# Kernel optimization log

Measured on AMD Instinct MI355X. Metric: run time of the kernel, lower is better.

## Reference

```python
import jax, jax.numpy as jnp
import numpy as np

B, R, C, NH = 8, 64, 256, 8
N = R * R            # 4096 tokens
HD = C // NH         # head dim 32
FF = 3               # focusing factor

def dwconv(x, w, b):
    # x: (B, C, H, W); w: (C, 1, kh, kw) depthwise
    y = jax.lax.conv_general_dilated(
        x, w, window_strides=(1, 1), padding='SAME',
        dimension_numbers=('NCHW', 'OIHW', 'NCHW'),
        feature_group_count=x.shape[1])
    return y + b[None, :, None, None]

def setup_inputs() -> dict:
    key = jax.random.key(0)
    ks = jax.random.split(key, 6)
    return {
        'qkv': jax.random.normal(ks[0], (3, B, N, C), jnp.float32),
        'pos_enc': jax.random.normal(ks[1], (1, N, C), jnp.float32) * 0.02,
        'scale': jax.random.normal(ks[2], (1, 1, C), jnp.float32) * 0.02,
        'w_v': jax.random.normal(ks[3], (C, 1, 3, 3), jnp.float32) * 0.1,
        'b_v': jnp.zeros((C,), jnp.float32),
        'w_dwc': jax.random.normal(ks[4], (HD, 1, 5, 5), jnp.float32) * 0.1,
        'b_dwc': jnp.zeros((HD,), jnp.float32),
    }

def reference(qkv, pos_enc, scale, w_v, b_v, w_dwc, b_dwc):
    q, k, v = qkv[0], qkv[1], qkv[2]          # each (B, N, C)
    # --- LePE: depthwise 3x3 conv on v over full channel dim ---
    v_img = v.transpose(0, 2, 1).reshape(B, C, R, R)
    lepe = dwconv(v_img, w_v, b_v)            # (B, C, R, R)
    lepe = lepe.reshape(B * NH, HD, N).transpose(0, 2, 1)   # (B*h, N, hd)
    v = v_img.reshape(B, C, N).transpose(0, 2, 1)           # (B, N, C)
    # --- focused kernelization ---
    k = k + pos_enc
    sc = jax.nn.softplus(scale)
    q = (jax.nn.relu(q) + 1e-6) / sc
    k = (jax.nn.relu(k) + 1e-6) / sc
    qn = jnp.linalg.norm(q, axis=-1, keepdims=True)
    kn = jnp.linalg.norm(k, axis=-1, keepdims=True)
    q = q ** FF
    k = k ** FF
    q = q / jnp.linalg.norm(q, axis=-1, keepdims=True) * qn
    k = k / jnp.linalg.norm(k, axis=-1, keepdims=True) * kn
    split = lambda x: x.reshape(B, N, NH, HD).transpose(0, 2, 1, 3).reshape(B * NH, N, HD)
    q, k, v = split(q), split(k), split(v)    # (B*h, N, hd)
    # --- linear attention (kv aggregation path: N >> hd) ---
    z = 1.0 / (jnp.einsum('bic,bc->bi', q, k.sum(axis=1)) + 1e-6)
    kv = jnp.einsum('bjc,bjd->bcd', k, v)     # (B*h, hd, hd)
    x = jnp.einsum('bic,bcd,bi->bid', q, kv, z)
    # --- dwc feature mixing on v per head ---
    fm = v.transpose(0, 2, 1).reshape(B * NH, HD, R, R)
    fm = dwconv(fm, w_dwc, b_dwc).reshape(B * NH, HD, N).transpose(0, 2, 1)
    x = x + fm + lepe
    x = x.reshape(B, NH, N, HD).transpose(0, 2, 1, 3).reshape(B, N, C)
    return x
```

## Files before the change

### kernel.cpp

```cpp
#include <hip/hip_runtime.h>
#include <math.h>

#define B_  8
#define R_  64
#define C_  256
#define NH_ 8
#define N_  4096
#define HD_ 32

__device__ __forceinline__ float softplus_rcp(float s) {
    return 1.f / __logf(1.f + __expf(s));
}

__global__ __launch_bounds__(256) void kernelN(
        const float* __restrict__ qkv, const float* __restrict__ pos,
        const float* __restrict__ scale,
        float* __restrict__ qs_arr, float* __restrict__ ks_arr) {
    const int t    = threadIdx.x;
    const int wave = t >> 6, lane = t & 63;
    const int tok  = blockIdx.x * 4 + wave;
    const int n    = tok & (N_ - 1);
    const int c0   = lane * 4;

    const size_t qidx = (size_t)tok * C_ + c0;
    const float4 q4 = *(const float4*)(qkv + qidx);
    const float4 k4 = *(const float4*)(qkv + (size_t)B_ * N_ * C_ + qidx);
    const float4 p4 = *(const float4*)(pos + (size_t)n * C_ + c0);
    const float4 s4 = *(const float4*)(scale + c0);

    float qa[4] = {q4.x, q4.y, q4.z, q4.w};
    float ka[4] = {k4.x, k4.y, k4.z, k4.w};
    float pa[4] = {p4.x, p4.y, p4.z, p4.w};
    float sa[4] = {s4.x, s4.y, s4.z, s4.w};

    float sq2 = 0.f, sq6 = 0.f, sk2 = 0.f, sk6 = 0.f;
    #pragma unroll
    for (int i = 0; i < 4; i++) {
        const float rsc = softplus_rcp(sa[i]);
        const float qv = (fmaxf(qa[i], 0.f) + 1e-6f) * rsc;
        const float kv = (fmaxf(ka[i] + pa[i], 0.f) + 1e-6f) * rsc;
        sq2 += qv * qv;  sk2 += kv * kv;
        const float q3 = qv * qv * qv, k3 = kv * kv * kv;
        sq6 += q3 * q3;  sk6 += k3 * k3;
    }
    #pragma unroll
    for (int m = 1; m < 64; m <<= 1) {
        sq2 += __shfl_xor(sq2, m, 64);
        sq6 += __shfl_xor(sq6, m, 64);
        sk2 += __shfl_xor(sk2, m, 64);
        sk6 += __shfl_xor(sk6, m, 64);
    }
    if (lane == 0) {
        qs_arr[tok] = sqrtf(sq2) * rsqrtf(sq6);
        ks_arr[tok] = sqrtf(sk2) * rsqrtf(sk6);
    }
}

__global__ __launch_bounds__(256) void kernelB2(
        const float* __restrict__ qkv, const float* __restrict__ pos,
        const float* __restrict__ scale, const float* __restrict__ ks_arr,
        float* __restrict__ kv_ws, float* __restrict__ ksum_ws) {
    __shared__ float k_s[128 * HD_];
    __shared__ float v_s[128 * HD_];
    __shared__ float rsc_s[HD_];
    const int t     = threadIdx.x;
    const int bh    = blockIdx.x >> 3;
    const int chunk = blockIdx.x & 7;
    const int b     = bh >> 3, h = bh & 7;
    const int c     = t >> 3, p = t & 7, dbase = p * 4;

    if (t < HD_) rsc_s[t] = softplus_rcp(scale[h * HD_ + t]);
    __syncthreads();

    float a0 = 0.f, a1 = 0.f, a2 = 0.f, a3 = 0.f, ksp = 0.f;
    const size_t kbase = (size_t)B_ * N_ * C_ + (size_t)b * N_ * C_ + h * HD_;
    const size_t vbase = (size_t)2 * B_ * N_ * C_ + (size_t)b * N_ * C_ + h * HD_;
    const int tokbase = b * N_;

    for (int tile = 0; tile < 4; tile++) {
        const int n0 = chunk * 512 + tile * 128;
        #pragma unroll
        for (int i = 0; i < 4; i++) {
            const int j  = (i * 256 + t) * 4;
            const int nl = j >> 5, d = j & 31;
            const float4 kr = *(const float4*)(qkv + kbase + (size_t)(n0 + nl) * C_ + d);
            const float4 pr = *(const float4*)(pos + (size_t)(n0 + nl) * C_ + h * HD_ + d);
            const float ksn = ks_arr[tokbase + n0 + nl];
            float4 o;
            {
                float v0 = (fmaxf(kr.x + pr.x, 0.f) + 1e-6f) * rsc_s[d + 0];
                float v1 = (fmaxf(kr.y + pr.y, 0.f) + 1e-6f) * rsc_s[d + 1];
                float v2 = (fmaxf(kr.z + pr.z, 0.f) + 1e-6f) * rsc_s[d + 2];
                float v3 = (fmaxf(kr.w + pr.w, 0.f) + 1e-6f) * rsc_s[d + 3];
                o.x = v0 * v0 * v0 * ksn;  o.y = v1 * v1 * v1 * ksn;
                o.z = v2 * v2 * v2 * ksn;  o.w = v3 * v3 * v3 * ksn;
            }
            *(float4*)&k_s[j] = o;
            ((float4*)v_s)[i * 256 + t] =
                *(const float4*)(qkv + vbase + (size_t)(n0 + nl) * C_ + d);
        }
        __syncthreads();
        #pragma unroll 4
        for (int nl = 0; nl < 128; nl++) {
            const float  kc = k_s[nl * HD_ + c];
            const float4 vv = *(const float4*)&v_s[nl * HD_ + dbase];
            a0 = fmaf(kc, vv.x, a0);
            a1 = fmaf(kc, vv.y, a1);
            a2 = fmaf(kc, vv.z, a2);
            a3 = fmaf(kc, vv.w, a3);
        }
        #pragma unroll
        for (int i = 0; i < 16; i++)
            ksp += k_s[(p + i * 8) * HD_ + c];
        __syncthreads();
    }
    float* kvdst = kv_ws + (size_t)bh * 1024 + c * HD_ + dbase;
    atomicAdd(kvdst + 0, a0);
    atomicAdd(kvdst + 1, a1);
    atomicAdd(kvdst + 2, a2);
    atomicAdd(kvdst + 3, a3);
    k_s[c * 8 + p] = ksp;
    __syncthreads();
    if (t < 32) {
        float s = 0.f;
        #pragma unroll
        for (int i = 0; i < 8; i++) s += k_s[t * 8 + i];
        atomicAdd(&ksum_ws[bh * HD_ + t], s);
    }
}

__global__ __launch_bounds__(256) void kernelCD2(
        const float* __restrict__ qkv, const float* __restrict__ qs_arr,
        const float* __restrict__ kv_ws, const float* __restrict__ ksum_ws,
        const float* __restrict__ scale,
        const float* __restrict__ w_v,  const float* __restrict__ b_v,
        const float* __restrict__ w_dwc, const float* __restrict__ b_dwc,
        float* __restrict__ out) {
    __shared__ float v_s[20 * 20 * 32];
    __shared__ float kv_s[1024];
    __shared__ float ks_s[32];
    __shared__ float rsc_s[32];
    const int t    = threadIdx.x;
    const int tile = blockIdx.x;
    const int h    = blockIdx.y;
    const int b    = blockIdx.z;
    const int ty0  = (tile >> 2) * 16, tx0 = (tile & 3) * 16;
    const int bh   = b * NH_ + h;

    ((float4*)kv_s)[t] = ((const float4*)(kv_ws + (size_t)bh * 1024))[t];
    if (t < 32) {
        ks_s[t]  = ksum_ws[bh * HD_ + t];
        rsc_s[t] = softplus_rcp(scale[h * HD_ + t]);
    }

    const float* vb = qkv + (size_t)2 * B_ * N_ * C_ + (size_t)b * N_ * C_ + h * HD_;
    #pragma unroll
    for (int i = 0; i < 13; i++) {
        const int idx = i * 256 + t;
        if (idx < 3200) {
            const int pix = idx >> 3, d4 = (idx & 7) * 4;
            const int yy = pix / 20, xx = pix - yy * 20;
            const int gy = ty0 + yy - 2, gx = tx0 + xx - 2;
            float4 val = make_float4(0.f, 0.f, 0.f, 0.f);
            if (gy >= 0 && gy < R_ && gx >= 0 && gx < R_)
                val = *(const float4*)(vb + (size_t)(gy * R_ + gx) * C_ + d4);
            *(float4*)&v_s[pix * 32 + d4] = val;
        }
    }

    const int c  = t & 31, pg = t >> 5;
    float wv[9], wd[25];
    {
        const float* wvp = w_v + (size_t)(h * HD_ + c) * 9;
        const float* wdp = w_dwc + (size_t)c * 25;
        #pragma unroll
        for (int i = 0; i < 9; i++)  wv[i] = wvp[i];
        #pragma unroll
        for (int i = 0; i < 25; i++) wd[i] = wdp[i];
    }
    const float bias = b_v[h * HD_ + c] + b_dwc[c];
    __syncthreads();

    float res[32];
    #pragma unroll
    for (int r2 = 0; r2 < 2; r2++) {
        const int ty = pg * 2 + r2;
        float win[5][5];
        #pragma unroll
        for (int j = 0; j < 5; j++)
            #pragma unroll
            for (int i = 0; i < 5; i++)
                win[j][i] = v_s[((ty + i) * 20 + j) * 32 + c];
        #pragma unroll
        for (int tx = 0; tx < 16; tx++) {
            float a = bias;
            #pragma unroll
            for (int j = 0; j < 5; j++) {
                const int slot = (tx + j) % 5;
                #pragma unroll
                for (int i = 0; i < 5; i++)
                    a = fmaf(wd[i * 5 + j], win[slot][i], a);
            }
            #pragma unroll
            for (int j = 1; j < 4; j++) {
                const int slot = (tx + j) % 5;
                #pragma unroll
                for (int i = 1; i < 4; i++)
                    a = fmaf(wv[(i - 1) * 3 + (j - 1)], win[slot][i], a);
            }
            res[r2 * 16 + tx] = a;
            if (tx < 15) {
                const int slot = tx % 5;
                #pragma unroll
                for (int i = 0; i < 5; i++)
                    win[slot][i] = v_s[((ty + i) * 20 + (tx + 5)) * 32 + c];
            }
        }
    }
    __syncthreads();
    #pragma unroll
    for (int r2 = 0; r2 < 2; r2++)
        #pragma unroll
        for (int tx = 0; tx < 16; tx++)
            v_s[((pg * 2 + r2) * 16 + tx) * 33 + c] = res[r2 * 16 + tx];
    __syncthreads();

    {
        const int tyy = t >> 4, txx = t & 15;
        const int n   = (ty0 + tyy) * R_ + (tx0 + txx);
        const int tok = b * N_ + n;
        float q[32];
        const float4* qsrc = (const float4*)(qkv + (size_t)tok * C_ + h * HD_);
        #pragma unroll
        for (int i = 0; i < 8; i++) ((float4*)q)[i] = qsrc[i];
        const float qs = qs_arr[tok];
        #pragma unroll
        for (int i = 0; i < 32; i++) {
            const float r = (fmaxf(q[i], 0.f) + 1e-6f) * rsc_s[i];
            q[i] = r * r * r * qs;
        }

        float denom = 1e-6f;
        #pragma unroll
        for (int cc = 0; cc < 32; cc++) denom = fmaf(q[cc], ks_s[cc], denom);
        const float z = 1.f / denom;

        float o[32];
        #pragma unroll
        for (int i = 0; i < 32; i++) o[i] = 0.f;
        #pragma unroll
        for (int cc = 0; cc < 32; cc++) {
            const float qc = q[cc];
            #pragma unroll
            for (int d = 0; d < 32; d++)
                o[d] = fmaf(qc, kv_s[cc * 32 + d], o[d]);
        }
        float4* dst = (float4*)(out + (size_t)tok * C_ + h * HD_);
        #pragma unroll
        for (int i = 0; i < 8; i++) {
            float4 v4;
            v4.x = fmaf(o[i*4+0], z, v_s[t * 33 + i*4+0]);
            v4.y = fmaf(o[i*4+1], z, v_s[t * 33 + i*4+1]);
            v4.z = fmaf(o[i*4+2], z, v_s[t * 33 + i*4+2]);
            v4.w = fmaf(o[i*4+3], z, v_s[t * 33 + i*4+3]);
            dst[i] = v4;
        }
    }
}

extern "C" void kernel_launch(void* const* d_in, const int* in_sizes, int n_in,
                              void* d_out, int out_size, void* d_ws, size_t ws_size,
                              hipStream_t stream) {
    const float* qkv   = (const float*)d_in[0];
    const float* pos   = (const float*)d_in[1];
    const float* scale = (const float*)d_in[2];
    const float* w_v   = (const float*)d_in[3];
    const float* b_v   = (const float*)d_in[4];
    const float* w_dwc = (const float*)d_in[5];
    const float* b_dwc = (const float*)d_in[6];
    float* out = (float*)d_out;

    float* qs_arr  = (float*)d_ws;
    float* ks_arr  = qs_arr + (size_t)B_ * N_;
    float* kv_ws   = ks_arr + (size_t)B_ * N_;
    float* ksum_ws = kv_ws + 64 * 1024;

    (void)hipMemsetAsync(kv_ws, 0, (64 * 1024 + 64 * 32) * sizeof(float), stream);
    kernelN<<<dim3(B_ * N_ / 4), 256, 0, stream>>>(qkv, pos, scale, qs_arr, ks_arr);
    kernelB2<<<dim3(512), 256, 0, stream>>>(qkv, pos, scale, ks_arr, kv_ws, ksum_ws);
    kernelCD2<<<dim3(16, NH_, B_), 256, 0, stream>>>(qkv, qs_arr, kv_ws, ksum_ws,
                                                     scale, w_v, b_v, w_dwc, b_dwc, out);
}
```

Before: 223.9 us.

## Fuse norm computation and kv aggregation into a single kernel

Merges the per-token norm kernel and the kv/ksum reduction kernel into one kernel that loads q, k, v and pos once per 64-token block, computes the focused k features in shared memory, and accumulates kv with a 4x8 register tile per thread. This removes a second global read of k and pos and the ks_arr round-trip, plus one launch. In exchange each thread issues many more global atomics, and the large shared-memory footprint may limit occupancy.

```diff
diff --git a/kernel.cpp b/kernel.cpp
--- a/kernel.cpp
+++ b/kernel.cpp
@@ -12,120 +12,128 @@
     return 1.f / __logf(1.f + __expf(s));
 }
 
-__global__ __launch_bounds__(256) void kernelN(
+__global__ __launch_bounds__(256) void kernelNB(
         const float* __restrict__ qkv, const float* __restrict__ pos,
         const float* __restrict__ scale,
-        float* __restrict__ qs_arr, float* __restrict__ ks_arr) {
+        float* __restrict__ qs_arr, float* __restrict__ kv_ws,
+        float* __restrict__ ksum_ws) {
+    __shared__ float kf_s[32 * C_];
+    __shared__ float v_s [32 * C_];
+    __shared__ float rsc_s[C_];
+    __shared__ float kred_s[4 * C_];
+
     const int t    = threadIdx.x;
     const int wave = t >> 6, lane = t & 63;
-    const int tok  = blockIdx.x * 4 + wave;
-    const int n    = tok & (N_ - 1);
     const int c0   = lane * 4;
-
-    const size_t qidx = (size_t)tok * C_ + c0;
-    const float4 q4 = *(const float4*)(qkv + qidx);
-    const float4 k4 = *(const float4*)(qkv + (size_t)B_ * N_ * C_ + qidx);
-    const float4 p4 = *(const float4*)(pos + (size_t)n * C_ + c0);
-    const float4 s4 = *(const float4*)(scale + c0);
-
-    float qa[4] = {q4.x, q4.y, q4.z, q4.w};
-    float ka[4] = {k4.x, k4.y, k4.z, k4.w};
-    float pa[4] = {p4.x, p4.y, p4.z, p4.w};
-    float sa[4] = {s4.x, s4.y, s4.z, s4.w};
-
-    float sq2 = 0.f, sq6 = 0.f, sk2 = 0.f, sk6 = 0.f;
-    #pragma unroll
-    for (int i = 0; i < 4; i++) {
-        const float rsc = softplus_rcp(sa[i]);
-        const float qv = (fmaxf(qa[i], 0.f) + 1e-6f) * rsc;
-        const float kv = (fmaxf(ka[i] + pa[i], 0.f) + 1e-6f) * rsc;
-        sq2 += qv * qv;  sk2 += kv * kv;
-        const float q3 = qv * qv * qv, k3 = kv * kv * kv;
-        sq6 += q3 * q3;  sk6 += k3 * k3;
-    }
-    #pragma unroll
-    for (int m = 1; m < 64; m <<= 1) {
-        sq2 += __shfl_xor(sq2, m, 64);
-        sq6 += __shfl_xor(sq6, m, 64);
-        sk2 += __shfl_xor(sk2, m, 64);
-        sk6 += __shfl_xor(sk6, m, 64);
-    }
-    if (lane == 0) {
-        qs_arr[tok] = sqrtf(sq2) * rsqrtf(sq6);
-        ks_arr[tok] = sqrtf(sk2) * rsqrtf(sk6);
-    }
-}
-
-__global__ __launch_bounds__(256) void kernelB2(
-        const float* __restrict__ qkv, const float* __restrict__ pos,
-        const float* __restrict__ scale, const float* __restrict__ ks_arr,
-        float* __restrict__ kv_ws, float* __restrict__ ksum_ws) {
-    __shared__ float k_s[128 * HD_];
-    __shared__ float v_s[128 * HD_];
-    __shared__ float rsc_s[HD_];
-    const int t     = threadIdx.x;
-    const int bh    = blockIdx.x >> 3;
-    const int chunk = blockIdx.x & 7;
-    const int b     = bh >> 3, h = bh & 7;
-    const int c     = t >> 3, p = t & 7, dbase = p * 4;
-
-    if (t < HD_) rsc_s[t] = softplus_rcp(scale[h * HD_ + t]);
-    __syncthreads();
-
-    float a0 = 0.f, a1 = 0.f, a2 = 0.f, a3 = 0.f, ksp = 0.f;
-    const size_t kbase = (size_t)B_ * N_ * C_ + (size_t)b * N_ * C_ + h * HD_;
-    const size_t vbase = (size_t)2 * B_ * N_ * C_ + (size_t)b * N_ * C_ + h * HD_;
-    const int tokbase = b * N_;
-
-    for (int tile = 0; tile < 4; tile++) {
-        const int n0 = chunk * 512 + tile * 128;
-        #pragma unroll
-        for (int i = 0; i < 4; i++) {
-            const int j  = (i * 256 + t) * 4;
-            const int nl = j >> 5, d = j & 31;
-            const float4 kr = *(const float4*)(qkv + kbase + (size_t)(n0 + nl) * C_ + d);
-            const float4 pr = *(const float4*)(pos + (size_t)(n0 + nl) * C_ + h * HD_ + d);
-            const float ksn = ks_arr[tokbase + n0 + nl];
-            float4 o;
-            {
-                float v0 = (fmaxf(kr.x + pr.x, 0.f) + 1e-6f) * rsc_s[d + 0];
-                float v1 = (fmaxf(kr.y + pr.y, 0.f) + 1e-6f) * rsc_s[d + 1];
-                float v2 = (fmaxf(kr.z + pr.z, 0.f) + 1e-6f) * rsc_s[d + 2];
-                float v3 = (fmaxf(kr.w + pr.w, 0.f) + 1e-6f) * rsc_s[d + 3];
-                o.x = v0 * v0 * v0 * ksn;  o.y = v1 * v1 * v1 * ksn;
-                o.z = v2 * v2 * v2 * ksn;  o.w = v3 * v3 * v3 * ksn;
-            }
-            *(float4*)&k_s[j] = o;
-            ((float4*)v_s)[i * 256 + t] =
-                *(const float4*)(qkv + vbase + (size_t)(n0 + nl) * C_ + d);
+    const int tok0 = blockIdx.x * 64;
+    const int b    = tok0 >> 12;
+
+    if (t < C_) rsc_s[t] = softplus_rcp(scale[t]);
+    __syncthreads();
+
+    const size_t qbase = (size_t)tok0 * C_;
+    const size_t kbase = (size_t)B_ * N_ * C_ + qbase;
+    const size_t vbase = (size_t)2 * B_ * N_ * C_ + qbase;
+
+    const int h  = t >> 5;
+    const int l  = t & 31;
+    const int cg = l & 7;
+    const int dg = l >> 3;
+
+    const float rs0 = rsc_s[c0 + 0], rs1 = rsc_s[c0 + 1];
+    const float rs2 = rsc_s[c0 + 2], rs3 = rsc_s[c0 + 3];
+
+    float acc[4][8];
+    #pragma unroll
+    for (int ii = 0; ii < 4; ii++)
+        #pragma unroll
+        for (int jj = 0; jj < 8; jj++) acc[ii][jj] = 0.f;
+    float ksp[4] = {0.f, 0.f, 0.f, 0.f};
+
+    for (int tile = 0; tile < 2; tile++) {
+        const int nb0 = tile * 32;
+        #pragma unroll
+        for (int i = 0; i < 8; i++) {
+            const int row = wave * 8 + i;
+            const int tok = tok0 + nb0 + row;
+            const int n   = tok & (N_ - 1);
+            const size_t off = (size_t)(nb0 + row) * C_ + c0;
+            const float4 q4 = *(const float4*)(qkv + qbase + off);
+            const float4 k4 = *(const float4*)(qkv + kbase + off);
+            const float4 v4 = *(const float4*)(qkv + vbase + off);
+            const float4 p4 = *(const float4*)(pos + (size_t)n * C_ + c0);
+
+            const float qv0 = (fmaxf(q4.x, 0.f) + 1e-6f) * rs0;
+            const float qv1 = (fmaxf(q4.y, 0.f) + 1e-6f) * rs1;
+            const float qv2 = (fmaxf(q4.z, 0.f) + 1e-6f) * rs2;
+            const float qv3 = (fmaxf(q4.w, 0.f) + 1e-6f) * rs3;
+            const float kw0 = (fmaxf(k4.x + p4.x, 0.f) + 1e-6f) * rs0;
+            const float kw1 = (fmaxf(k4.y + p4.y, 0.f) + 1e-6f) * rs1;
+            const float kw2 = (fmaxf(k4.z + p4.z, 0.f) + 1e-6f) * rs2;
+            const float kw3 = (fmaxf(k4.w + p4.w, 0.f) + 1e-6f) * rs3;
+
+            const float q30 = qv0 * qv0 * qv0, q31 = qv1 * qv1 * qv1;
+            const float q32 = qv2 * qv2 * qv2, q33 = qv3 * qv3 * qv3;
+            const float k30 = kw0 * kw0 * kw0, k31 = kw1 * kw1 * kw1;
+            const float k32 = kw2 * kw2 * kw2, k33 = kw3 * kw3 * kw3;
+
+            float sq2 = qv0 * qv0 + qv1 * qv1 + qv2 * qv2 + qv3 * qv3;
+            float sq6 = q30 * q30 + q31 * q31 + q32 * q32 + q33 * q33;
+            float sk2 = kw0 * kw0 + kw1 * kw1 + kw2 * kw2 + kw3 * kw3;
+            float sk6 = k30 * k30 + k31 * k31 + k32 * k32 + k33 * k33;
+            #pragma unroll
+            for (int m = 1; m < 64; m <<= 1) {
+                sq2 += __shfl_xor(sq2, m, 64);
+                sq6 += __shfl_xor(sq6, m, 64);
+                sk2 += __shfl_xor(sk2, m, 64);
+                sk6 += __shfl_xor(sk6, m, 64);
+            }
+            if (lane == 0) qs_arr[tok] = sqrtf(sq2) * rsqrtf(sq6);
+            const float ks = sqrtf(sk2) * rsqrtf(sk6);
+
+            float4 kf;
+            kf.x = k30 * ks;  kf.y = k31 * ks;
+            kf.z = k32 * ks;  kf.w = k33 * ks;
+            *(float4*)&kf_s[row * C_ + c0] = kf;
+            *(float4*)&v_s [row * C_ + c0] = v4;
+            ksp[0] += kf.x;  ksp[1] += kf.y;
+            ksp[2] += kf.z;  ksp[3] += kf.w;
         }
         __syncthreads();
-        #pragma unroll 4
-        for (int nl = 0; nl < 128; nl++) {
-            const float  kc = k_s[nl * HD_ + c];
-            const float4 vv = *(const float4*)&v_s[nl * HD_ + dbase];
-            a0 = fmaf(kc, vv.x, a0);
-            a1 = fmaf(kc, vv.y, a1);
-            a2 = fmaf(kc, vv.z, a2);
-            a3 = fmaf(kc, vv.w, a3);
-        }
-        #pragma unroll
-        for (int i = 0; i < 16; i++)
-            ksp += k_s[(p + i * 8) * HD_ + c];
+        {
+            const float* kfp = kf_s + h * HD_ + cg * 4;
+            const float* vp  = v_s  + h * HD_ + dg * 8;
+            #pragma unroll 8
+            for (int nl = 0; nl < 32; nl++) {
+                const float4 kr = *(const float4*)(kfp + nl * C_);
+                const float4 va = *(const float4*)(vp  + nl * C_);
+                const float4 vb = *(const float4*)(vp  + nl * C_ + 4);
+                const float kk[4] = {kr.x, kr.y, kr.z, kr.w};
+                const float vv[8] = {va.x, va.y, va.z, va.w,
+                                     vb.x, vb.y, vb.z, vb.w};
+                #pragma unroll
+                for (int ii = 0; ii < 4; ii++)
+                    #pragma unroll
+                    for (int jj = 0; jj < 8; jj++)
+                        acc[ii][jj] = fmaf(kk[ii], vv[jj], acc[ii][jj]);
+            }
+        }
         __syncthreads();
     }
-    float* kvdst = kv_ws + (size_t)bh * 1024 + c * HD_ + dbase;
-    atomicAdd(kvdst + 0, a0);
-    atomicAdd(kvdst + 1, a1);
-    atomicAdd(kvdst + 2, a2);
-    atomicAdd(kvdst + 3, a3);
-    k_s[c * 8 + p] = ksp;
-    __syncthreads();
-    if (t < 32) {
-        float s = 0.f;
-        #pragma unroll
-        for (int i = 0; i < 8; i++) s += k_s[t * 8 + i];
-        atomicAdd(&ksum_ws[bh * HD_ + t], s);
+
+    float* kvdst = kv_ws + (size_t)(b * NH_ + h) * 1024 + (cg * 4) * HD_ + dg * 8;
+    #pragma unroll
+    for (int ii = 0; ii < 4; ii++)
+        #pragma unroll
+        for (int jj = 0; jj < 8; jj++)
+            atomicAdd(kvdst + ii * HD_ + jj, acc[ii][jj]);
+
+    *(float4*)&kred_s[wave * C_ + c0] = make_float4(ksp[0], ksp[1], ksp[2], ksp[3]);
+    __syncthreads();
+    if (t < C_) {
+        const float s = kred_s[t] + kred_s[C_ + t] + kred_s[2 * C_ + t]
+                      + kred_s[3 * C_ + t];
+        atomicAdd(&ksum_ws[b * C_ + t], s);
     }
 }
 
@@ -281,13 +289,11 @@
     float* out = (float*)d_out;
 
     float* qs_arr  = (float*)d_ws;
-    float* ks_arr  = qs_arr + (size_t)B_ * N_;
-    float* kv_ws   = ks_arr + (size_t)B_ * N_;
+    float* kv_ws   = qs_arr + (size_t)B_ * N_;
     float* ksum_ws = kv_ws + 64 * 1024;
 
     (void)hipMemsetAsync(kv_ws, 0, (64 * 1024 + 64 * 32) * sizeof(float), stream);
-    kernelN<<<dim3(B_ * N_ / 4), 256, 0, stream>>>(qkv, pos, scale, qs_arr, ks_arr);
-    kernelB2<<<dim3(512), 256, 0, stream>>>(qkv, pos, scale, ks_arr, kv_ws, ksum_ws);
+    kernelNB<<<dim3(512), 256, 0, stream>>>(qkv, pos, scale, qs_arr, kv_ws, ksum_ws);
     kernelCD2<<<dim3(16, NH_, B_), 256, 0, stream>>>(qkv, qs_arr, kv_ws, ksum_ws,
                                                      scale, w_v, b_v, w_dwc, b_dwc, out);
 }
```

New measurement: 317.6 us. 1.42x slower.
